# Optimization experiments

Measured on AMD Instinct MI355X. Metric: run time of the kernel, lower is better.

Reference implementation:

```python
import jax, jax.numpy as jnp
import numpy as np

B = 8_388_608
GRID = 201   # floor(lat/0.9) in [-100,100], floor(lon/1.8) in [-100,100]
OFFSET = 100
ALPHA = 0.1


def setup_inputs() -> dict:
    key = jax.random.key(0)
    k1, k2, k3 = jax.random.split(key, 3)
    predictions = jax.random.uniform(k1, (B, 2), dtype=jnp.float32)
    labels = jax.random.uniform(k2, (B, 2), dtype=jnp.float32)
    weight_grid = jax.random.uniform(k3, (GRID, GRID), dtype=jnp.float32)
    return {"predictions": predictions, "labels": labels, "weight_grid": weight_grid}


def reference(predictions, labels, weight_grid):
    # |pred - label| (the code calls it mse_error but computes abs error)
    err = jnp.abs(predictions - labels)                       # [B, 2]
    # denormalize: lat in [-90, 90), lon in [-180, 180)
    lat = predictions[..., 0] * 180.0 - 90.0
    lon = predictions[..., 1] * 360.0 - 180.0
    # torch float // is floor division; indices offset into dense grid
    xi = jnp.floor(lat / 0.9).astype(jnp.int32) + OFFSET
    yi = jnp.floor(lon / 1.8).astype(jnp.int32) + OFFSET
    xi = jnp.clip(xi, 0, GRID - 1)
    yi = jnp.clip(yi, 0, GRID - 1)
    w = weight_grid[xi, yi]                                   # [B]
    weighted = err + err * (ALPHA - ALPHA * w[:, None])       # [B, 2]
    return weighted.mean()
```

## Files before the change

### kernel.cpp

```cpp
#include <hip/hip_runtime.h>
#include <hip/hip_fp16.h>


constexpr int   GRIDN  = 201;
constexpr int   GRIDSZ = GRIDN * GRIDN;
constexpr float ALPHA  = 0.1f;

__global__ __launch_bounds__(1024, 8) void wmse_reduce(
    const float4* __restrict__ pred4,
    const float4* __restrict__ lab4,
    const float*  __restrict__ wg,
    float*        __restrict__ out,
    int n4, float scale)
{
    __shared__ __half wg_lds[GRIDSZ];

    const float4* wg4 = (const float4*)wg;
    for (int j = threadIdx.x; j < GRIDSZ / 4; j += 1024) {
        const float4 v = wg4[j];
        __half2 h01, h23;
        h01.x = __float2half(v.x); h01.y = __float2half(v.y);
        h23.x = __float2half(v.z); h23.y = __float2half(v.w);
        *reinterpret_cast<__half2*>(&wg_lds[j * 4])     = h01;
        *reinterpret_cast<__half2*>(&wg_lds[j * 4 + 2]) = h23;
    }
    if (threadIdx.x == 0)
        wg_lds[GRIDSZ - 1] = __float2half(wg[GRIDSZ - 1]);
    __syncthreads();

    float acc = 0.0f;
    const int stride = gridDim.x * blockDim.x;
    #pragma unroll 4
    for (int i = blockIdx.x * blockDim.x + threadIdx.x; i < n4; i += stride) {
        const float4 p = pred4[i];
        const float4 l = lab4[i];

        {
            const float e = fabsf(p.x - l.x) + fabsf(p.y - l.y);
            int xi = min(max((int)(p.x * 200.0f), 0), GRIDN - 1);
            int yi = min(max((int)(p.y * 200.0f), 0), GRIDN - 1);
            const float w = __half2float(wg_lds[xi * GRIDN + yi]);
            acc += e * fmaf(-ALPHA, w, 1.0f + ALPHA);
        }
        {
            const float e = fabsf(p.z - l.z) + fabsf(p.w - l.w);
            int xi = min(max((int)(p.z * 200.0f), 0), GRIDN - 1);
            int yi = min(max((int)(p.w * 200.0f), 0), GRIDN - 1);
            const float w = __half2float(wg_lds[xi * GRIDN + yi]);
            acc += e * fmaf(-ALPHA, w, 1.0f + ALPHA);
        }
    }

    #pragma unroll
    for (int off = 32; off > 0; off >>= 1)
        acc += __shfl_down(acc, off, 64);

    __shared__ float red[16];
    const int lane = threadIdx.x & 63;
    const int wid  = threadIdx.x >> 6;
    if (lane == 0) red[wid] = acc;
    __syncthreads();
    if (threadIdx.x == 0) {
        float s = 0.0f;
        #pragma unroll
        for (int k = 0; k < 16; ++k) s += red[k];
        atomicAdd(out, s * scale);
    }
}

extern "C" void kernel_launch(void* const* d_in, const int* in_sizes, int n_in,
                              void* d_out, int out_size, void* d_ws, size_t ws_size,
                              hipStream_t stream) {
    const float4* pred = (const float4*)d_in[0];
    const float4* lab  = (const float4*)d_in[1];
    const float*  wg   = (const float*)d_in[2];
    float*        out  = (float*)d_out;

    const long long total = (long long)in_sizes[0];
    const int   n4    = (int)(total / 4);
    const float scale = 1.0f / (float)total;

    hipMemsetAsync(d_out, 0, sizeof(float), stream);

    const int block = 1024;
    const int grid  = 512;
    wmse_reduce<<<grid, block, 0, stream>>>(pred, lab, wg, out, n4, scale);
}
```

Before: 153.8 us.

## Use nontemporal loads and two-pass partial reduction instead of memset plus atomics

Input streams are now read with nontemporal loads so they bypass cache retention. The memset and the per-block atomicAdd are replaced by per-block partial sums written to workspace, followed by a small second kernel that reduces the 512 partials. This removes the memset launch and atomic contention but adds a second kernel launch.

```diff
diff --git a/kernel.cpp b/kernel.cpp
--- a/kernel.cpp
+++ b/kernel.cpp
@@ -2,22 +2,24 @@
 #include <hip/hip_fp16.h>
 
 
+typedef float f32x4 __attribute__((ext_vector_type(4)));
+
 constexpr int   GRIDN  = 201;
 constexpr int   GRIDSZ = GRIDN * GRIDN;
 constexpr float ALPHA  = 0.1f;
+constexpr int   NBLK   = 512;
 
-__global__ __launch_bounds__(1024, 8) void wmse_reduce(
-    const float4* __restrict__ pred4,
-    const float4* __restrict__ lab4,
-    const float*  __restrict__ wg,
-    float*        __restrict__ out,
-    int n4, float scale)
+__global__ __launch_bounds__(1024, 8) void wmse_partial(
+    const f32x4* __restrict__ pred4,
+    const f32x4* __restrict__ lab4,
+    const float* __restrict__ wg,
+    float*       __restrict__ partials,
+    int n4)
 {
     __shared__ __half wg_lds[GRIDSZ];
 
-    const float4* wg4 = (const float4*)wg;
     for (int j = threadIdx.x; j < GRIDSZ / 4; j += 1024) {
-        const float4 v = wg4[j];
+        const f32x4 v = ((const f32x4*)wg)[j];
         __half2 h01, h23;
         h01.x = __float2half(v.x); h01.y = __float2half(v.y);
         h23.x = __float2half(v.z); h23.y = __float2half(v.w);
@@ -32,8 +34,8 @@
     const int stride = gridDim.x * blockDim.x;
     #pragma unroll 4
     for (int i = blockIdx.x * blockDim.x + threadIdx.x; i < n4; i += stride) {
-        const float4 p = pred4[i];
-        const float4 l = lab4[i];
+        const f32x4 p = __builtin_nontemporal_load(&pred4[i]);
+        const f32x4 l = __builtin_nontemporal_load(&lab4[i]);
 
         {
             const float e = fabsf(p.x - l.x) + fabsf(p.y - l.y);
@@ -64,25 +66,43 @@
         float s = 0.0f;
         #pragma unroll
         for (int k = 0; k < 16; ++k) s += red[k];
-        atomicAdd(out, s * scale);
+        partials[blockIdx.x] = s;
+    }
+}
+
+__global__ __launch_bounds__(512) void wmse_final(
+    const float* __restrict__ partials, float* __restrict__ out, float scale)
+{
+    float v = partials[threadIdx.x];
+    #pragma unroll
+    for (int off = 32; off > 0; off >>= 1)
+        v += __shfl_down(v, off, 64);
+    __shared__ float red[8];
+    const int lane = threadIdx.x & 63;
+    const int wid  = threadIdx.x >> 6;
+    if (lane == 0) red[wid] = v;
+    __syncthreads();
+    if (threadIdx.x == 0) {
+        float s = 0.0f;
+        #pragma unroll
+        for (int k = 0; k < 8; ++k) s += red[k];
+        out[0] = s * scale;
     }
 }
 
 extern "C" void kernel_launch(void* const* d_in, const int* in_sizes, int n_in,
                               void* d_out, int out_size, void* d_ws, size_t ws_size,
                               hipStream_t stream) {
-    const float4* pred = (const float4*)d_in[0];
-    const float4* lab  = (const float4*)d_in[1];
-    const float*  wg   = (const float*)d_in[2];
-    float*        out  = (float*)d_out;
+    const f32x4* pred = (const f32x4*)d_in[0];
+    const f32x4* lab  = (const f32x4*)d_in[1];
+    const float* wg   = (const float*)d_in[2];
+    float*       out  = (float*)d_out;
+    float*       part = (float*)d_ws;
 
     const long long total = (long long)in_sizes[0];
     const int   n4    = (int)(total / 4);
     const float scale = 1.0f / (float)total;
 
-    hipMemsetAsync(d_out, 0, sizeof(float), stream);
-
-    const int block = 1024;
-    const int grid  = 512;
-    wmse_reduce<<<grid, block, 0, stream>>>(pred, lab, wg, out, n4, scale);
+    wmse_partial<<<NBLK, 1024, 0, stream>>>(pred, lab, wg, part, n4);
+    wmse_final<<<1, 512, 0, stream>>>(part, out, scale);
 }
```

Measured after the change: 143.0 us. 7.0% less time.
